# Optimization experiments

Measured on AMD Instinct MI355X. Metric: run time of the kernel, lower is better.

Reference implementation:

```python
import jax, jax.numpy as jnp
import numpy as np

V, B, NP, NJ = 5, 32, 20, 17
NB = 16
ND = 128
POSE_MIN_DEPTH, POSE_MAX_DEPTH = 2000.0, 8000.0
POSE_SIGMA = 100.0
KS = 11
HIDDEN_ROUGH, HIDDEN = 1024, 1024
BONES = np.array([[0,1],[0,2],[1,3],[2,4],[5,6],[5,7],[7,9],[6,8],[8,10],[5,11],[6,12],[11,12],[11,13],[13,15],[12,14],[14,16]], dtype=np.int32)


def setup_inputs() -> dict:
    key = jax.random.key(0)
    ks = jax.random.split(key, 12)
    wh = jnp.array([1920.0, 1080.0], jnp.float32)
    kpts = jax.random.uniform(ks[0], (V, B, NP, NJ, 2), jnp.float32) * wh
    pose_vis = jnp.ones((V, B, NP), jnp.float32)
    joint_vis = (jax.random.uniform(ks[1], (V, B, NP, NJ)) > 0.15).astype(jnp.float32)
    gt_pose_depths = jax.random.uniform(ks[2], (B, NP), jnp.float32, 2000.0, 8000.0)
    gt_joint_depths = jax.random.uniform(ks[3], (B, NP, NJ), jnp.float32, -100.0, 100.0)
    angles = np.linspace(-0.3, 0.3, V)
    Rs = np.stack([np.array([[np.cos(a), 0.0, np.sin(a)], [0.0, 1.0, 0.0], [-np.sin(a), 0.0, np.cos(a)]], dtype=np.float32) for a in angles])
    cam_R = jnp.broadcast_to(jnp.asarray(Rs)[:, None], (V, B, 3, 3))
    tvec = np.zeros((V, 3), np.float32); tvec[:, 0] = np.linspace(-500.0, 500.0, V)
    cam_T = jnp.broadcast_to(jnp.asarray(tvec)[:, None], (V, B, 3))
    cam_f = jnp.full((V, B, 2), 1400.0, jnp.float32)
    cam_c = jnp.broadcast_to(jnp.array([960.0, 540.0], jnp.float32), (V, B, 2))
    image_wh = jnp.broadcast_to(jnp.array([1920.0, 1080.0], jnp.float32), (V, B, 2))
    num_persons = jax.random.randint(ks[4], (V, B), 10, NP + 1, jnp.int32)
    Wr1 = jax.random.normal(ks[5], (HIDDEN_ROUGH, NJ * 2)) * 0.02
    br1 = jnp.zeros((HIDDEN_ROUGH,), jnp.float32)
    Wr2 = jax.random.normal(ks[6], (NJ, HIDDEN_ROUGH)) * 0.02
    br2 = jnp.zeros((NJ,), jnp.float32)
    Wc1 = jax.random.normal(ks[7], (HIDDEN, NJ + NB, 3)) * 0.02
    bc1 = jnp.zeros((HIDDEN,), jnp.float32)
    Wc2 = jax.random.normal(ks[8], (1, HIDDEN, 3)) * 0.02
    bc2 = jnp.zeros((1,), jnp.float32)
    bones = jnp.asarray(BONES)
    return dict(kpts=kpts, pose_vis=pose_vis, joint_vis=joint_vis, gt_pose_depths=gt_pose_depths, gt_joint_depths=gt_joint_depths, cam_R=cam_R, cam_T=cam_T, cam_f=cam_f, cam_c=cam_c, image_wh=image_wh, num_persons=num_persons, Wr1=Wr1, br1=br1, Wr2=Wr2, br2=br2, Wc1=Wc1, bc1=bc1, Wc2=Wc2, bc2=bc2, bones=bones)


def _bone_len(p, bones):
    # p: [B, Np, Nj, D, 2] -> [B, Np, Nb, D]
    a = p[:, :, bones[:, 0]]
    b = p[:, :, bones[:, 1]]
    return jnp.sqrt(jnp.sum((a - b) ** 2, -1) + 1e-12)


def _conv1d(x, w, b):
    # x [N,C,L], w [O,I,3]
    y = jax.lax.conv_general_dilated(x, w, (1,), 'SAME', dimension_numbers=('NCH', 'OIH', 'NCH'))
    return y + b[None, :, None]


def _forward(kpts, joint_vis, cam_R, cam_T, cam_f, cam_c, image_wh, num_persons, Wr1, br1, Wr2, br2, Wc1, bc1, Wc2, bc2, bones):
    V_, B_, NP_, NJ_, _ = kpts.shape
    labels = jnp.arange(ND, dtype=jnp.float32) / (ND - 1) * (POSE_MAX_DEPTH - POSE_MIN_DEPTH) + POSE_MIN_DEPTH
    kt = kpts[0]  # target-view 2D poses [B,Np,Nj,2]
    # faithful to original indexing quirk: normalize all batches by batch-0 image size
    kn = kt / image_wh[0, 0][None, None, None, :]
    x = kn.reshape(B_ * NP_, NJ_ * 2)
    h = jax.nn.relu(x @ Wr1.T + br1)
    rough = (h @ Wr2.T + br2).reshape(B_, NP_, NJ_) * 1000.0
    rough = jax.lax.stop_gradient(rough)  # .detach() in original
    depths = labels[None, None, None, :] + rough[..., None]  # [B,Np,Nj,D]
    # back-project target 2D poses at every depth hypothesis
    R0, T0, f0, c0 = cam_R[0], cam_T[0], cam_f[0], cam_c[0]
    uvn = (kt - c0[:, None, None, :]) / f0[:, None, None, :]
    xy = uvn[..., None, :] * depths[..., None]
    cam_pts = jnp.concatenate([xy, depths[..., None]], -1)
    p3d = jnp.einsum('bji,bpkdj->bpkdi', R0, cam_pts) + T0[:, None, None, None, :]  # world [B,Np,Nj,D,3]

    scores = scores2 = boundings = boundings2 = None
    for rv in range(1, V_):
        Rr, Tr, fr, cr = cam_R[rv], cam_T[rv], cam_f[rv], cam_c[rv]
        xc = jnp.einsum('bij,bpkdj->bpkdi', Rr, p3d - Tr[:, None, None, None, :])
        p2t = xc[..., :2] / (xc[..., 2:3] + 1e-8) * fr[:, None, None, None, :] + cr[:, None, None, None, :]
        pr = kpts[rv]         # [B,Npr,Nj,2]
        vr = joint_vis[rv]    # [B,Npr,Nj]
        # pairwise dist over (target-person, ref-person) per joint/depth
        d = jnp.sum((p2t[:, :, None] - pr[:, None, :, :, None, :]) ** 2, -1)  # [B,Npt,Npr,Nj,D]
        w = vr[:, None, :, :, None]
        pdist = jnp.sum(d * w, 3) / (jnp.sum(w, 3) + 1e-8)  # [B,Npt,Npr,D]
        valid = jnp.arange(NP_)[None, None, :, None] < num_persons[rv][:, None, None, None]
        pdist = jnp.where(valid, pdist, 1e5)
        mm = jnp.argmin(pdist, 2)  # [B,Npt,D] nearest ref pose
        bidx = jnp.arange(B_)[:, None, None]
        matched = jnp.transpose(pr[bidx, mm], (0, 1, 3, 2, 4))  # [B,Npt,Nj,D,2]
        mvis = jnp.transpose(vr[bidx, mm], (0, 1, 3, 2))        # [B,Npt,Nj,D]
        mdist = jnp.sum((p2t - matched) ** 2, -1)
        score = jnp.exp(-jnp.sqrt(mdist + 1e-12) / POSE_SIGMA)  # panoptic branch
        score_bl = jnp.exp(-jnp.abs(_bone_len(matched, bones) - _bone_len(p2t, bones)) / 5.0)
        wimg = image_wh[rv][:, None, None, None, 0]
        himg = image_wh[rv][:, None, None, None, 1]
        inb = ((p2t[..., 0] >= 0) & (p2t[..., 1] >= 0) & (p2t[..., 0] <= wimg - 1) & (p2t[..., 1] <= himg - 1)).astype(score.dtype)
        bounding = inb * mvis
        bounding2 = jnp.broadcast_to(mvis[:, :, :1, :], score_bl.shape)
        if scores is None:
            scores, scores2 = score * bounding, score_bl * bounding2
            boundings, boundings2 = bounding, bounding2
        else:
            scores = scores + score * bounding
            scores2 = scores2 + score_bl * bounding2
            boundings = boundings + bounding
            boundings2 = boundings2 + bounding2
    psv = (scores / (boundings + 1e-8)).reshape(B_ * NP_, NJ_, ND)
    psv2 = (scores2 / (boundings2 + 1e-8)).reshape(B_ * NP_, NB, ND)
    xin = jnp.concatenate([psv, psv2], 1)  # [BN, Nj+Nb, D]
    hc = jax.nn.relu(_conv1d(xin, Wc1, bc1))
    logits = _conv1d(hc, Wc2, bc2)[:, 0, :]  # [BN, D]
    vol = jax.nn.softmax(logits, -1)
    # soft-argmax restricted to a window around the argmax
    pos = jnp.arange(ND, dtype=vol.dtype)
    idx = jnp.argmax(vol, -1)
    mask = (jnp.abs(pos[None, :] - idx[:, None].astype(vol.dtype)) <= KS // 2).astype(vol.dtype)
    mv = vol * mask
    mv = mv / (jnp.sum(mv, -1, keepdims=True) + 1e-8)
    pred_idx = jnp.sum(mv * pos, -1).reshape(B_, NP_)
    return pred_idx / (ND - 1) * (POSE_MAX_DEPTH - POSE_MIN_DEPTH) + POSE_MIN_DEPTH


def reference(kpts, pose_vis, joint_vis, gt_pose_depths, gt_joint_depths, cam_R, cam_T, cam_f, cam_c, image_wh, num_persons, Wr1, br1, Wr2, br2, Wc1, bc1, Wc2, bc2, bones):
    return _forward(kpts, joint_vis, cam_R, cam_T, cam_f, cam_c, image_wh, num_persons, Wr1, br1, Wr2, br2, Wc1, bc1, Wc2, bc2, bones)
```

## Files before the change

kernel.cpp:

```cpp
#include <hip/hip_runtime.h>
#include <math.h>

#define VV  5
#define BB  32
#define NPP 20
#define NJJ 17
#define NBB 16
#define NDD 128
#define HID 1024
#define KPITCH 128
#define KSTEPS 7
#define PRP 36
#define VRP 20
#define NCH 34
#define A_T_ELEMS (32 * KSTEPS * 64 * 8)
#define EPI_ELEMS (32 * 4 * 64 * 16)

typedef __attribute__((ext_vector_type(8))) short short8;
typedef __attribute__((ext_vector_type(16))) float float16;

static constexpr int BONE_A[NBB] = {0,0,1,2,5,5,7,6,8,5,6,11,11,13,12,14};
static constexpr int BONE_B[NBB] = {1,2,3,4,6,7,9,8,10,11,12,12,13,15,14,16};

__device__ __forceinline__ float warp_red_sum(float v) {
#pragma unroll
  for (int off = 32; off >= 1; off >>= 1) v += __shfl_xor(v, off, 64);
  return v;
}

__global__ __launch_bounds__(256) void prep_kernel(
    const float* __restrict__ Wc1, const float* __restrict__ Wc2,
    const float* __restrict__ bc1,
    unsigned short* __restrict__ A_hi, unsigned short* __restrict__ A_lo,
    float* __restrict__ epi) {
  int gidx = blockIdx.x * 256 + threadIdx.x;
  if (gidx < A_T_ELEMS) {
    int e = gidx & 7;
    int l = (gidx >> 3) & 63;
    int rest = gidx >> 9;
    int ks = rest % 7;
    int ot = rest / 7;
    int o = ot * 32 + (l & 31);
    int kk = ks * 16 + (l >> 5) * 8 + e;
    float x = (kk < 99) ? Wc1[o * 99 + kk] : 0.0f;
    unsigned int u = __float_as_uint(x);
    unsigned short hi = (unsigned short)(u >> 16);
    float xh = __uint_as_float((u >> 16) << 16);
    unsigned short lo = (unsigned short)(__float_as_uint(x - xh) >> 16);
    A_hi[gidx] = hi;
    A_lo[gidx] = lo;
  } else {
    int idx2 = gidx - A_T_ELEMS;
    if (idx2 < EPI_ELEMS) {
      int c = idx2 & 15;
      int l = (idx2 >> 4) & 63;
      int rb = (idx2 >> 10) & 3;
      int ot = idx2 >> 12;
      int base = ot * 32 + 4 * (l >> 5) + 8 * rb;
      epi[idx2] = (c < 12) ? Wc2[base * 3 + c] : bc1[base + (c - 12)];
    }
  }
}

__global__ __launch_bounds__(512, 4) void pose_front_kernel(
    const float* __restrict__ kpts, const float* __restrict__ joint_vis,
    const float* __restrict__ cam_R, const float* __restrict__ cam_T,
    const float* __restrict__ cam_f, const float* __restrict__ cam_c,
    const float* __restrict__ image_wh, const int* __restrict__ num_persons,
    const float* __restrict__ Wr1, const float* __restrict__ br1,
    const float* __restrict__ Wr2, const float* __restrict__ br2,
    float* __restrict__ ws_partial) {
  const int n = blockIdx.x;
  const int b = n / NPP;
  const int p = n % NPP;
  const int tid = threadIdx.x;
  const int wv = tid >> 6, ln = tid & 63;
  const int rvv = tid >> 7;
  const int d   = tid & (NDD - 1);

  __shared__ float sh_x[NJJ * 2];
  __shared__ float sh_h[HID];
  __shared__ float sh_rough[NJJ];
  __shared__ float sh_base[NJJ][3];
  __shared__ __align__(16) float sh_pr[4][NPP][PRP];
  __shared__ __align__(16) float sh_vr[4][NPP][VRP];

  if (tid < NJJ * 2) {
    int j = tid >> 1, c = tid & 1;
    float k = kpts[((size_t)(b * NPP + p)) * NJJ * 2 + j * 2 + c];
    sh_x[tid] = k / image_wh[c];
  }
  __syncthreads();

#pragma unroll
  for (int k = 0; k < 2; ++k) {
    int m = tid + k * 512;
    float acc = br1[m];
#pragma unroll
    for (int c = 0; c < NJJ * 2; ++c) acc = fmaf(Wr1[m * (NJJ * 2) + c], sh_x[c], acc);
    sh_h[m] = fmaxf(acc, 0.0f);
  }
  __syncthreads();

  for (int j = wv; j < NJJ; j += 8) {
    float part = 0.0f;
    for (int m = ln; m < HID; m += 64) part = fmaf(Wr2[j * HID + m], sh_h[m], part);
    part = warp_red_sum(part);
    if (ln == 0) sh_rough[j] = (part + br2[j]) * 1000.0f;
  }
  if (tid < NJJ) {
    int j = tid;
    const float* R0 = cam_R + (size_t)b * 9;
    float c0x = cam_c[b * 2 + 0], c0y = cam_c[b * 2 + 1];
    float f0x = cam_f[b * 2 + 0], f0y = cam_f[b * 2 + 1];
    float kx = kpts[((size_t)(b * NPP + p)) * NJJ * 2 + j * 2 + 0];
    float ky = kpts[((size_t)(b * NPP + p)) * NJJ * 2 + j * 2 + 1];
    float ux = (kx - c0x) / f0x;
    float uy = (ky - c0y) / f0y;
#pragma unroll
    for (int i = 0; i < 3; ++i)
      sh_base[j][i] = R0[0 * 3 + i] * ux + R0[1 * 3 + i] * uy + R0[2 * 3 + i];
  }
#pragma unroll
  for (int rr = 0; rr < 4; ++rr) {
    const float* prg = kpts + ((size_t)(rr + 1) * BB + b) * NPP * NJJ * 2;
    for (int idx = tid; idx < NPP * NJJ * 2; idx += 512)
      sh_pr[rr][idx / 34][idx % 34] = prg[idx];
    const float* vrg = joint_vis + ((size_t)(rr + 1) * BB + b) * NPP * NJJ;
    for (int idx = tid; idx < NPP * NJJ; idx += 512)
      sh_vr[rr][idx / 17][idx % 17] = vrg[idx];
  }
  if (tid < 4 * BB) {
    int rr = tid >> 5, q = tid & 31;
    if (q < NPP) {
      sh_pr[rr][q][34] = 0.0f; sh_pr[rr][q][35] = 0.0f;
      sh_vr[rr][q][17] = 0.0f; sh_vr[rr][q][18] = 0.0f; sh_vr[rr][q][19] = 0.0f;
    }
  }
  __syncthreads();

  {
    const int rv = rvv + 1;
    const int vb = rv * BB + b;
    const float* Rr = cam_R + (size_t)vb * 9;
    const float R00 = Rr[0], R01 = Rr[1], R02 = Rr[2];
    const float R10 = Rr[3], R11 = Rr[4], R12 = Rr[5];
    const float R20 = Rr[6], R21 = Rr[7], R22 = Rr[8];
    const float Trx = cam_T[vb * 3 + 0], Try = cam_T[vb * 3 + 1], Trz = cam_T[vb * 3 + 2];
    const float frx = cam_f[vb * 2 + 0], fry = cam_f[vb * 2 + 1];
    const float crx = cam_c[vb * 2 + 0], cry = cam_c[vb * 2 + 1];
    const float wmax = image_wh[vb * 2 + 0] - 1.0f;
    const float hmax = image_wh[vb * 2 + 1] - 1.0f;
    const int nprv = num_persons[vb];
    const float T0x = cam_T[b * 3 + 0], T0y = cam_T[b * 3 + 1], T0z = cam_T[b * 3 + 2];
    const float lab = ((float)d / 127.0f) * 6000.0f + 2000.0f;

    float px[NJJ], py[NJJ];
#pragma unroll
    for (int j = 0; j < NJJ; ++j) {
      float dep = lab + sh_rough[j];
      float p0 = fmaf(dep, sh_base[j][0], T0x);
      float p1 = fmaf(dep, sh_base[j][1], T0y);
      float p2 = fmaf(dep, sh_base[j][2], T0z);
      float q0 = p0 - Trx, q1 = p1 - Try, q2 = p2 - Trz;
      float xc0 = R00 * q0 + R01 * q1 + R02 * q2;
      float xc1 = R10 * q0 + R11 * q1 + R12 * q2;
      float xc2 = R20 * q0 + R21 * q1 + R22 * q2 + 1e-8f;
      px[j] = xc0 / xc2 * frx + crx;
      py[j] = xc1 / xc2 * fry + cry;
    }

    float best = 3.4e38f;
    int mm = 0;
#pragma unroll 1
    for (int q = 0; q < NPP; ++q) {
      const float4* pr4 = (const float4*)(&sh_pr[rvv][q][0]);
      const float4* vr4 = (const float4*)(&sh_vr[rvv][q][0]);
      float num = 0.0f, den = 0.0f;
#pragma unroll
      for (int g4 = 0; g4 < 4; ++g4) {
        float4 w  = vr4[g4];
        float4 pa = pr4[2 * g4 + 0];
        float4 pb = pr4[2 * g4 + 1];
        { float dx = px[4*g4+0] - pa.x, dy = py[4*g4+0] - pa.y; num = fmaf(w.x, dx*dx + dy*dy, num); den += w.x; }
        { float dx = px[4*g4+1] - pa.z, dy = py[4*g4+1] - pa.w; num = fmaf(w.y, dx*dx + dy*dy, num); den += w.y; }
        { float dx = px[4*g4+2] - pb.x, dy = py[4*g4+2] - pb.y; num = fmaf(w.z, dx*dx + dy*dy, num); den += w.z; }
        { float dx = px[4*g4+3] - pb.z, dy = py[4*g4+3] - pb.w; num = fmaf(w.w, dx*dx + dy*dy, num); den += w.w; }
      }
      {
        float w16 = sh_vr[rvv][q][16];
        float4 pc = pr4[8];
        float dx = px[16] - pc.x, dy = py[16] - pc.y;
        num = fmaf(w16, dx*dx + dy*dy, num); den += w16;
      }
      float pd = num / (den + 1e-8f);
      if (q >= nprv) pd = 100000.0f;
      if (pd < best) { best = pd; mm = q; }
    }

    float* pbase = ws_partial + (((size_t)n * NCH) * 4 + rvv) * 128 + d;
    unsigned int maskB = 0u;
#pragma unroll
    for (int j = 0; j < NJJ; ++j) {
      float mx = sh_pr[rvv][mm][j * 2 + 0];
      float my = sh_pr[rvv][mm][j * 2 + 1];
      float mv = sh_vr[rvv][mm][j];
      float dx = px[j] - mx, dy = py[j] - my;
      float sc = expf(-sqrtf(dx * dx + dy * dy + 1e-12f) / 100.0f);
      float inb = (px[j] >= 0.0f && py[j] >= 0.0f && px[j] <= wmax && py[j] <= hmax) ? 1.0f : 0.0f;
      float bd = inb * mv;
      pbase[j * 512] = sc * bd;
      maskB |= ((unsigned int)(bd != 0.0f)) << j;
    }
    float v0 = sh_vr[rvv][mm][0];
    maskB |= ((unsigned int)(v0 != 0.0f)) << 17;
#pragma unroll
    for (int nb = 0; nb < NBB; ++nb) {
      const int a = BONE_A[nb], c = BONE_B[nb];
      float ax = sh_pr[rvv][mm][a * 2 + 0], ay = sh_pr[rvv][mm][a * 2 + 1];
      float cx = sh_pr[rvv][mm][c * 2 + 0], cy = sh_pr[rvv][mm][c * 2 + 1];
      float dmx = ax - cx, dmy = ay - cy;
      float blm = sqrtf(dmx * dmx + dmy * dmy + 1e-12f);
      float dpx = px[a] - px[c], dpy = py[a] - py[c];
      float blp = sqrtf(dpx * dpx + dpy * dpy + 1e-12f);
      float scb = expf(-fabsf(blm - blp) / 5.0f);
      pbase[(NJJ + nb) * 512] = scb * v0;
    }
    *(unsigned int*)(pbase + 33 * 512) = maskB;
  }
}

__global__ __launch_bounds__(128) void reduce_kernel(
    const float* __restrict__ ws_partial, float* __restrict__ ws_xin) {
  const int n = blockIdx.x;
  const int t = threadIdx.x;
  const float* pb = ws_partial + ((size_t)n * NCH) * 4 * 128;
  float* xo = ws_xin + (size_t)n * (NJJ + NBB) * NDD;

  unsigned int m0 = __float_as_uint(pb[(33 * 4 + 0) * 128 + t]);
  unsigned int m1 = __float_as_uint(pb[(33 * 4 + 1) * 128 + t]);
  unsigned int m2 = __float_as_uint(pb[(33 * 4 + 2) * 128 + t]);
  unsigned int m3 = __float_as_uint(pb[(33 * 4 + 3) * 128 + t]);

#pragma unroll
  for (int i = 0; i < NJJ; ++i) {
    const float* a = pb + (i * 4) * 128 + t;
    float s = ((a[0] + a[128]) + a[256]) + a[384];
    int bj = ((m0 >> i) & 1) + ((m1 >> i) & 1) + ((m2 >> i) & 1) + ((m3 >> i) & 1);
    xo[i * NDD + t] = s / ((float)bj + 1e-8f);
  }
  int b2 = ((m0 >> 17) & 1) + ((m1 >> 17) & 1) + ((m2 >> 17) & 1) + ((m3 >> 17) & 1);
  float den2 = (float)b2 + 1e-8f;
#pragma unroll
  for (int nb = 0; nb < NBB; ++nb) {
    const float* a = pb + ((NJJ + nb) * 4) * 128 + t;
    float s = ((a[0] + a[128]) + a[256]) + a[384];
    xo[(NJJ + nb) * NDD + t] = s / den2;
  }
}

__global__ __launch_bounds__(512, 2) void conv_mfma_kernel(
    const float* __restrict__ ws_xin,
    const unsigned short* __restrict__ A_hi, const unsigned short* __restrict__ A_lo,
    const float* __restrict__ epi,
    const float* __restrict__ bc2, float* __restrict__ out) {
  const int n = blockIdx.x;
  const int tid = threadIdx.x;
  const int w = tid >> 6;
  const int l = tid & 63;
  const int lrow = l & 31;
  const int g = l >> 5;

  __shared__ __align__(16) unsigned short bT_hi[128 * KPITCH];
  __shared__ __align__(16) unsigned short bT_lo[128 * KPITCH];
  __shared__ float plg[3][8][NDD];
  __shared__ float sh_l[NDD];
  __shared__ float sh_e[NDD];
  __shared__ float sh_sc[2];

  for (int i = tid; i < 3 * 8 * NDD; i += 512) ((float*)plg)[i] = 0.0f;

  const float* xn = ws_xin + (size_t)n * (NJJ + NBB) * NDD;
  for (int idx = tid; idx < 64 * 128; idx += 512) {
    const int kp = (idx & 63) << 1;
    const int t  = idx >> 6;
    unsigned int hp = 0, lp = 0;
#pragma unroll
    for (int u = 0; u < 2; ++u) {
      const int kk = kp + u;
      float x = 0.0f;
      if (kk < 99) {
        int i3 = kk / 3;
        int k3 = kk - i3 * 3;
        int tt = t + k3 - 1;
        if (tt >= 0 && tt < 128) x = xn[i3 * NDD + tt];
      }
      unsigned int uu = __float_as_uint(x);
      unsigned int hi = uu >> 16;
      float xh = __uint_as_float(hi << 16);
      unsigned int lo = __float_as_uint(x - xh) >> 16;
      hp |= hi << (16 * u);
      lp |= lo << (16 * u);
    }
    const int e = t * KPITCH + (kp ^ ((t & 15) << 3));
    *(unsigned int*)(bT_hi + e) = hp;
    *(unsigned int*)(bT_lo + e) = lp;
  }
  __syncthreads();

#pragma unroll 1
  for (int otile = 0; otile < 4; ++otile) {
    const int otg = w * 4 + otile;

    short8 Ah[KSTEPS], Al[KSTEPS];
    {
      const short8* ahT = ((const short8*)A_hi) + (size_t)otg * KSTEPS * 64 + l;
      const short8* alT = ((const short8*)A_lo) + (size_t)otg * KSTEPS * 64 + l;
#pragma unroll
      for (int ks = 0; ks < KSTEPS; ++ks) {
        Ah[ks] = ahT[ks * 64];
        Al[ks] = alT[ks * 64];
      }
    }
    float w2f[48];
    float bcf[16];
#pragma unroll
    for (int rb = 0; rb < 4; ++rb) {
      const float4* ep = ((const float4*)epi) + ((size_t)(otg * 4 + rb) * 64 + l) * 4;
      float4 e0 = ep[0], e1 = ep[1], e2 = ep[2], e3 = ep[3];
      w2f[rb * 12 + 0] = e0.x;  w2f[rb * 12 + 1] = e0.y;  w2f[rb * 12 + 2] = e0.z;
      w2f[rb * 12 + 3] = e0.w;  w2f[rb * 12 + 4] = e1.x;  w2f[rb * 12 + 5] = e1.y;
      w2f[rb * 12 + 6] = e1.z;  w2f[rb * 12 + 7] = e1.w;  w2f[rb * 12 + 8] = e2.x;
      w2f[rb * 12 + 9] = e2.y;  w2f[rb * 12 + 10] = e2.z; w2f[rb * 12 + 11] = e2.w;
      bcf[rb * 4 + 0] = e3.x; bcf[rb * 4 + 1] = e3.y;
      bcf[rb * 4 + 2] = e3.z; bcf[rb * 4 + 3] = e3.w;
    }

#pragma unroll 1
    for (int ttile = 0; ttile < 4; ++ttile) {
      const int trow = ttile * 32 + lrow;
      const unsigned short* brh = bT_hi + trow * KPITCH;
      const unsigned short* brl = bT_lo + trow * KPITCH;
      const int sw = (trow & 15) << 3;

      float16 X, Y;
#pragma unroll
      for (int r = 0; r < 16; ++r) { X[r] = 0.0f; Y[r] = 0.0f; }

#pragma unroll
      for (int ks = 0; ks < KSTEPS; ++ks) {
        const int e = (ks * 16 + g * 8) ^ sw;
        short8 bh = *(const short8*)(brh + e);
        X = __builtin_amdgcn_mfma_f32_32x32x16_bf16(Ah[ks], bh, X, 0, 0, 0);
        Y = __builtin_amdgcn_mfma_f32_32x32x16_bf16(Al[ks], bh, Y, 0, 0, 0);
      }
#pragma unroll
      for (int ks = 0; ks < KSTEPS; ++ks) {
        const int e = (ks * 16 + g * 8) ^ sw;
        short8 bl = *(const short8*)(brl + e);
        if (ks & 1) Y = __builtin_amdgcn_mfma_f32_32x32x16_bf16(Ah[ks], bl, Y, 0, 0, 0);
        else        X = __builtin_amdgcn_mfma_f32_32x32x16_bf16(Ah[ks], bl, X, 0, 0, 0);
      }

      float sP = 0.0f, sC = 0.0f, sM = 0.0f;
#pragma unroll
      for (int r = 0; r < 16; ++r) {
        float h = fmaxf((X[r] + Y[r]) + bcf[(r >> 2) * 4 + (r & 3)], 0.0f);
        sP = fmaf(h, w2f[(r >> 2) * 12 + (r & 3) * 3 + 0], sP);
        sC = fmaf(h, w2f[(r >> 2) * 12 + (r & 3) * 3 + 1], sC);
        sM = fmaf(h, w2f[(r >> 2) * 12 + (r & 3) * 3 + 2], sM);
      }
      sP += __shfl_xor(sP, 32, 64);
      sC += __shfl_xor(sC, 32, 64);
      sM += __shfl_xor(sM, 32, 64);
      if (l < 32) {
        plg[0][w][trow] += sP;
        plg[1][w][trow] += sC;
        plg[2][w][trow] += sM;
      }
    }
  }
  __syncthreads();

  if (tid < NDD) {
    int t = tid;
    float lg = bc2[0];
#pragma unroll
    for (int ww = 0; ww < 8; ++ww) lg += plg[1][ww][t];
    if (t > 0) {
#pragma unroll
      for (int ww = 0; ww < 8; ++ww) lg += plg[0][ww][t - 1];
    }
    if (t < NDD - 1) {
#pragma unroll
      for (int ww = 0; ww < 8; ++ww) lg += plg[2][ww][t + 1];
    }
    sh_l[t] = lg;
  }
  __syncthreads();
  if (tid < 64) {
    float v1 = sh_l[tid], v2 = sh_l[tid + 64];
    float mv; int mi;
    if (v2 > v1) { mv = v2; mi = tid + 64; } else { mv = v1; mi = tid; }
#pragma unroll
    for (int off = 32; off >= 1; off >>= 1) {
      float ov = __shfl_xor(mv, off, 64);
      int   oi = __shfl_xor(mi, off, 64);
      if (ov > mv || (ov == mv && oi < mi)) { mv = ov; mi = oi; }
    }
    if (tid == 0) { sh_sc[0] = mv; ((int*)sh_sc)[1] = mi; }
  }
  __syncthreads();
  const float gmax = sh_sc[0];
  const int gidx = ((const int*)sh_sc)[1];
  if (tid < NDD) sh_e[tid] = expf(sh_l[tid] - gmax);
  __syncthreads();
  if (tid < 64) {
    float S = warp_red_sum(sh_e[tid] + sh_e[tid + 64]);
    float a1 = 0.0f, a2 = 0.0f;
#pragma unroll
    for (int k = 0; k < 2; ++k) {
      int t = tid + k * 64;
      float vol = sh_e[t] / S;
      float msk = (fabsf((float)t - (float)gidx) <= 5.0f) ? 1.0f : 0.0f;
      float mvv = vol * msk;
      a1 += mvv;
      a2 += mvv * (float)t;
    }
    a1 = warp_red_sum(a1);
    a2 = warp_red_sum(a2);
    if (tid == 0) {
      float pred = a2 / (a1 + 1e-8f);
      out[n] = pred / 127.0f * 6000.0f + 2000.0f;
    }
  }
}

extern "C" void kernel_launch(void* const* d_in, const int* in_sizes, int n_in,
                              void* d_out, int out_size, void* d_ws, size_t ws_size,
                              hipStream_t stream) {
  (void)in_sizes; (void)n_in; (void)out_size; (void)ws_size;
  const float* kpts        = (const float*)d_in[0];
  const float* joint_vis   = (const float*)d_in[2];
  const float* cam_R       = (const float*)d_in[5];
  const float* cam_T       = (const float*)d_in[6];
  const float* cam_f       = (const float*)d_in[7];
  const float* cam_c       = (const float*)d_in[8];
  const float* image_wh    = (const float*)d_in[9];
  const int*   num_persons = (const int*)d_in[10];
  const float* Wr1 = (const float*)d_in[11];
  const float* br1 = (const float*)d_in[12];
  const float* Wr2 = (const float*)d_in[13];
  const float* br2 = (const float*)d_in[14];
  const float* Wc1 = (const float*)d_in[15];
  const float* bc1 = (const float*)d_in[16];
  const float* Wc2 = (const float*)d_in[17];
  const float* bc2 = (const float*)d_in[18];
  float* out = (float*)d_out;

  unsigned short* A_hi = (unsigned short*)d_ws;
  unsigned short* A_lo = A_hi + A_T_ELEMS;
  float* epi        = (float*)(A_lo + A_T_ELEMS);
  float* ws_xin     = epi + EPI_ELEMS;
  float* ws_partial = ws_xin + (size_t)BB * NPP * (NJJ + NBB) * NDD;

  const int prep_items = A_T_ELEMS + EPI_ELEMS;
  hipLaunchKernelGGL(prep_kernel, dim3((prep_items + 255) / 256), dim3(256), 0, stream,
                     Wc1, Wc2, bc1, A_hi, A_lo, epi);
  hipLaunchKernelGGL(pose_front_kernel, dim3(BB * NPP), dim3(512), 0, stream,
                     kpts, joint_vis, cam_R, cam_T, cam_f, cam_c, image_wh,
                     num_persons, Wr1, br1, Wr2, br2, ws_partial);
  hipLaunchKernelGGL(reduce_kernel, dim3(BB * NPP), dim3(128), 0, stream,
                     ws_partial, ws_xin);
  hipLaunchKernelGGL(conv_mfma_kernel, dim3(BB * NPP), dim3(512), 0, stream,
                     ws_xin, A_hi, A_lo, epi, bc2, out);
}
```

Measured before the change: 181.7 us.

## Split pose front kernel into rough-depth MLP and per-depth matching kernels

Splits the fused front kernel into a 256-thread kernel that computes the rough-depth MLP and the back-projection base rays, writing them to workspace, and a matching kernel launched with twice as many 256-thread blocks, each handling half of the depth bins. This shrinks the per-block register and shared footprint and spreads the matching work over more blocks to improve occupancy. In exchange it adds a kernel launch, a global round trip for the rough and base values, and reloads the other-view keypoints once per half-block.

```diff
diff --git a/kernel.cpp b/kernel.cpp
--- a/kernel.cpp
+++ b/kernel.cpp
@@ -13,6 +13,8 @@
 #define PRP 36
 #define VRP 20
 #define NCH 34
+#define RGH_P 20
+#define BASE_P 52
 #define A_T_ELEMS (32 * KSTEPS * 64 * 8)
 #define EPI_ELEMS (32 * 4 * 64 * 16)
 
@@ -62,28 +64,21 @@
   }
 }
 
-__global__ __launch_bounds__(512, 4) void pose_front_kernel(
-    const float* __restrict__ kpts, const float* __restrict__ joint_vis,
-    const float* __restrict__ cam_R, const float* __restrict__ cam_T,
+__global__ __launch_bounds__(256) void pose_pre_kernel(
+    const float* __restrict__ kpts, const float* __restrict__ cam_R,
     const float* __restrict__ cam_f, const float* __restrict__ cam_c,
-    const float* __restrict__ image_wh, const int* __restrict__ num_persons,
+    const float* __restrict__ image_wh,
     const float* __restrict__ Wr1, const float* __restrict__ br1,
     const float* __restrict__ Wr2, const float* __restrict__ br2,
-    float* __restrict__ ws_partial) {
+    float* __restrict__ ws_rough, float* __restrict__ ws_base) {
   const int n = blockIdx.x;
   const int b = n / NPP;
   const int p = n % NPP;
   const int tid = threadIdx.x;
   const int wv = tid >> 6, ln = tid & 63;
-  const int rvv = tid >> 7;
-  const int d   = tid & (NDD - 1);
 
   __shared__ float sh_x[NJJ * 2];
   __shared__ float sh_h[HID];
-  __shared__ float sh_rough[NJJ];
-  __shared__ float sh_base[NJJ][3];
-  __shared__ __align__(16) float sh_pr[4][NPP][PRP];
-  __shared__ __align__(16) float sh_vr[4][NPP][VRP];
 
   if (tid < NJJ * 2) {
     int j = tid >> 1, c = tid & 1;
@@ -93,8 +88,8 @@
   __syncthreads();
 
 #pragma unroll
-  for (int k = 0; k < 2; ++k) {
-    int m = tid + k * 512;
+  for (int k = 0; k < 4; ++k) {
+    int m = tid + k * 256;
     float acc = br1[m];
 #pragma unroll
     for (int c = 0; c < NJJ * 2; ++c) acc = fmaf(Wr1[m * (NJJ * 2) + c], sh_x[c], acc);
@@ -102,12 +97,13 @@
   }
   __syncthreads();
 
-  for (int j = wv; j < NJJ; j += 8) {
+  for (int j = wv; j < NJJ; j += 4) {
     float part = 0.0f;
     for (int m = ln; m < HID; m += 64) part = fmaf(Wr2[j * HID + m], sh_h[m], part);
     part = warp_red_sum(part);
-    if (ln == 0) sh_rough[j] = (part + br2[j]) * 1000.0f;
-  }
+    if (ln == 0) ws_rough[(size_t)n * RGH_P + j] = (part + br2[j]) * 1000.0f;
+  }
+
   if (tid < NJJ) {
     int j = tid;
     const float* R0 = cam_R + (size_t)b * 9;
@@ -119,15 +115,42 @@
     float uy = (ky - c0y) / f0y;
 #pragma unroll
     for (int i = 0; i < 3; ++i)
-      sh_base[j][i] = R0[0 * 3 + i] * ux + R0[1 * 3 + i] * uy + R0[2 * 3 + i];
-  }
+      ws_base[(size_t)n * BASE_P + j * 3 + i] =
+          R0[0 * 3 + i] * ux + R0[1 * 3 + i] * uy + R0[2 * 3 + i];
+  }
+}
+
+__global__ __launch_bounds__(256, 4) void pose_match_kernel(
+    const float* __restrict__ kpts, const float* __restrict__ joint_vis,
+    const float* __restrict__ cam_R, const float* __restrict__ cam_T,
+    const float* __restrict__ cam_f, const float* __restrict__ cam_c,
+    const float* __restrict__ image_wh, const int* __restrict__ num_persons,
+    const float* __restrict__ ws_rough, const float* __restrict__ ws_base,
+    float* __restrict__ ws_partial) {
+  const int bid = blockIdx.x;
+  const int n = bid >> 1;
+  const int bh = bid & 1;
+  const int b = n / NPP;
+  const int tid = threadIdx.x;
+  const int rvv = tid >> 6;
+  const int d = bh * 64 + (tid & 63);
+
+  __shared__ float sh_rough[NJJ];
+  __shared__ float sh_base[NJJ][3];
+  __shared__ __align__(16) float sh_pr[4][NPP][PRP];
+  __shared__ __align__(16) float sh_vr[4][NPP][VRP];
+
+  if (tid < NJJ) sh_rough[tid] = ws_rough[(size_t)n * RGH_P + tid];
+  if (tid >= 64 && tid < 64 + NJJ * 3)
+    ((float*)sh_base)[tid - 64] = ws_base[(size_t)n * BASE_P + (tid - 64)];
+
 #pragma unroll
   for (int rr = 0; rr < 4; ++rr) {
     const float* prg = kpts + ((size_t)(rr + 1) * BB + b) * NPP * NJJ * 2;
-    for (int idx = tid; idx < NPP * NJJ * 2; idx += 512)
+    for (int idx = tid; idx < NPP * NJJ * 2; idx += 256)
       sh_pr[rr][idx / 34][idx % 34] = prg[idx];
     const float* vrg = joint_vis + ((size_t)(rr + 1) * BB + b) * NPP * NJJ;
-    for (int idx = tid; idx < NPP * NJJ; idx += 512)
+    for (int idx = tid; idx < NPP * NJJ; idx += 256)
       sh_vr[rr][idx / 17][idx % 17] = vrg[idx];
   }
   if (tid < 4 * BB) {
@@ -350,16 +373,16 @@
 #pragma unroll
       for (int ks = 0; ks < KSTEPS; ++ks) {
         const int e = (ks * 16 + g * 8) ^ sw;
-        short8 bh = *(const short8*)(brh + e);
-        X = __builtin_amdgcn_mfma_f32_32x32x16_bf16(Ah[ks], bh, X, 0, 0, 0);
-        Y = __builtin_amdgcn_mfma_f32_32x32x16_bf16(Al[ks], bh, Y, 0, 0, 0);
+        short8 bh8 = *(const short8*)(brh + e);
+        X = __builtin_amdgcn_mfma_f32_32x32x16_bf16(Ah[ks], bh8, X, 0, 0, 0);
+        Y = __builtin_amdgcn_mfma_f32_32x32x16_bf16(Al[ks], bh8, Y, 0, 0, 0);
       }
 #pragma unroll
       for (int ks = 0; ks < KSTEPS; ++ks) {
         const int e = (ks * 16 + g * 8) ^ sw;
-        short8 bl = *(const short8*)(brl + e);
-        if (ks & 1) Y = __builtin_amdgcn_mfma_f32_32x32x16_bf16(Ah[ks], bl, Y, 0, 0, 0);
-        else        X = __builtin_amdgcn_mfma_f32_32x32x16_bf16(Ah[ks], bl, X, 0, 0, 0);
+        short8 bl8 = *(const short8*)(brl + e);
+        if (ks & 1) Y = __builtin_amdgcn_mfma_f32_32x32x16_bf16(Ah[ks], bl8, Y, 0, 0, 0);
+        else        X = __builtin_amdgcn_mfma_f32_32x32x16_bf16(Ah[ks], bl8, X, 0, 0, 0);
       }
 
       float sP = 0.0f, sC = 0.0f, sM = 0.0f;
@@ -463,13 +486,18 @@
   float* epi        = (float*)(A_lo + A_T_ELEMS);
   float* ws_xin     = epi + EPI_ELEMS;
   float* ws_partial = ws_xin + (size_t)BB * NPP * (NJJ + NBB) * NDD;
+  float* ws_rough   = ws_partial + (size_t)BB * NPP * NCH * 4 * 128;
+  float* ws_base    = ws_rough + (size_t)BB * NPP * RGH_P;
 
   const int prep_items = A_T_ELEMS + EPI_ELEMS;
   hipLaunchKernelGGL(prep_kernel, dim3((prep_items + 255) / 256), dim3(256), 0, stream,
                      Wc1, Wc2, bc1, A_hi, A_lo, epi);
-  hipLaunchKernelGGL(pose_front_kernel, dim3(BB * NPP), dim3(512), 0, stream,
+  hipLaunchKernelGGL(pose_pre_kernel, dim3(BB * NPP), dim3(256), 0, stream,
+                     kpts, cam_R, cam_f, cam_c, image_wh, Wr1, br1, Wr2, br2,
+                     ws_rough, ws_base);
+  hipLaunchKernelGGL(pose_match_kernel, dim3(BB * NPP * 2), dim3(256), 0, stream,
                      kpts, joint_vis, cam_R, cam_T, cam_f, cam_c, image_wh,
-                     num_persons, Wr1, br1, Wr2, br2, ws_partial);
+                     num_persons, ws_rough, ws_base, ws_partial);
   hipLaunchKernelGGL(reduce_kernel, dim3(BB * NPP), dim3(128), 0, stream,
                      ws_partial, ws_xin);
   hipLaunchKernelGGL(conv_mfma_kernel, dim3(BB * NPP), dim3(512), 0, stream,
```

Result: slower. 188.8 us (+3.9%).
